# Optimization experiments

Measured on AMD Instinct MI355X. Metric: run time of the kernel, lower is better.

## Reference

```python
import jax, jax.numpy as jnp
import numpy as np

N, E = 3000, 96000
IN_C, HID, OUT_C = 512, 256, 64
K1, K2, K3 = 2000, 1000, 500  # ceil(ratio * n) per depth; ratios = [2000/N, 0.5, 0.5]


def gcn_conv(A, x, W, b):
    # GCNConv(improved=True): A_hat = A + 2I, symmetric norm; A[i, j] = weight of edge j -> i
    n = A.shape[0]
    Ah = A + 2.0 * jnp.eye(n, dtype=A.dtype)
    deg = Ah.sum(axis=1)
    dis = jnp.where(deg > 0, jax.lax.rsqrt(deg), 0.0)
    return (dis[:, None] * Ah * dis[None, :]) @ (x @ W) + b


def augment(A):
    # GraphUNet.augment_adj: add self loops, A @ A (spspmm), remove self loops
    n = A.shape[0]
    eye = jnp.eye(n, dtype=A.dtype)
    Ah = A + eye
    return (Ah @ Ah) * (1.0 - eye)


def topk_pool(A, x, w, k):
    # TopKPooling: score = tanh((x @ w) / ||w||); keep top-k nodes, scale feats, take sub-adjacency
    score = jnp.tanh((x @ w) / jnp.linalg.norm(w))
    sv, perm = jax.lax.top_k(score, k)
    return x[perm] * sv[:, None], A[perm][:, perm], perm


def setup_inputs():
    key = jax.random.key(0)
    ks = jax.random.split(key, 16)

    def glorot(k, shape):
        lim = float(np.sqrt(6.0 / (shape[0] + shape[1])))
        return jax.random.uniform(k, shape, jnp.float32, -lim, lim)

    return {
        "x": jax.random.normal(ks[0], (N, IN_C), jnp.float32),
        "edge_index": jax.random.randint(ks[1], (2, E), 0, N, jnp.int32),
        "W0": glorot(ks[2], (IN_C, HID)), "b0": jnp.zeros((HID,), jnp.float32),
        "W1": glorot(ks[3], (HID, HID)), "b1": jnp.zeros((HID,), jnp.float32),
        "W2": glorot(ks[4], (HID, HID)), "b2": jnp.zeros((HID,), jnp.float32),
        "W3": glorot(ks[5], (HID, HID)), "b3": jnp.zeros((HID,), jnp.float32),
        "p1": jax.random.normal(ks[6], (HID,), jnp.float32),
        "p2": jax.random.normal(ks[7], (HID,), jnp.float32),
        "p3": jax.random.normal(ks[8], (HID,), jnp.float32),
        "U0": glorot(ks[9], (HID, HID)), "c0": jnp.zeros((HID,), jnp.float32),
        "U1": glorot(ks[10], (HID, HID)), "c1": jnp.zeros((HID,), jnp.float32),
        "U2": glorot(ks[11], (HID, OUT_C)), "c2": jnp.zeros((OUT_C,), jnp.float32),
    }


def reference(x, edge_index, W0, b0, W1, b1, W2, b2, W3, b3, p1, p2, p3, U0, c0, U1, c1, U2, c2):
    # eval mode: dropout_edge(p=0.2) and F.dropout(p=0.92) are identity
    relu = jax.nn.relu
    src, dst = edge_index[0], edge_index[1]
    A = jnp.zeros((N, N), x.dtype).at[dst, src].add(1.0)  # dense adjacency, coalesces duplicates

    x0 = relu(gcn_conv(A, x, W0, b0))                     # down conv 0 on original graph
    x1in, A1, perm1 = topk_pool(augment(A), x0, p1, K1)
    x1 = relu(gcn_conv(A1, x1in, W1, b1))
    x2in, A2, perm2 = topk_pool(augment(A1), x1, p2, K2)
    x2 = relu(gcn_conv(A2, x2in, W2, b2))
    x3in, A3, perm3 = topk_pool(augment(A2), x2, p3, K3)
    x3 = relu(gcn_conv(A3, x3in, W3, b3))

    h = x2 + jnp.zeros_like(x2).at[perm3].set(x3)         # unpool + sum residual
    h = relu(gcn_conv(A2, h, U0, c0))
    h = x1 + jnp.zeros_like(x1).at[perm2].set(h)
    h = relu(gcn_conv(A1, h, U1, c1))
    h = x0 + jnp.zeros_like(x0).at[perm1].set(h)
    h = gcn_conv(A, h, U2, c2)                            # final up conv, no activation
    return jax.nn.log_softmax(h, axis=1)
```

## Files before the change

### kernel.cpp

```cpp
#include <hip/hip_runtime.h>
#include <math.h>
#include <stdint.h>

#define N0   3000
#define NE   96000
#define INC  512
#define HIDF 256
#define OUTC 64
#define KP1  2000
#define KP2  1000
#define KP3  500
#define KP1P 2048
#define KP2P 1024
#define KP3P 512

typedef __bf16 bf16x8 __attribute__((ext_vector_type(8)));
typedef float f32x4 __attribute__((ext_vector_type(4)));

#define GLDS16(gp, lp)                                                   \
  __builtin_amdgcn_global_load_lds(                                      \
      (__attribute__((address_space(1))) void*)(gp),                     \
      (__attribute__((address_space(3))) void*)(lp), 16, 0, 0)

static __global__ void count_k(const int* __restrict__ ei, int* __restrict__ cd) {
  int e = blockIdx.x * blockDim.x + threadIdx.x;
  if (e < NE) atomicAdd(&cd[ei[NE + e]], 1);
}

static __global__ __launch_bounds__(1024) void scan_excl_k(const int* __restrict__ cnt,
                                                           int* __restrict__ start, int n,
                                                           float* __restrict__ dis0) {
  __shared__ int s[4096];
  int tid = threadIdx.x;
  for (int i = tid; i < 4096; i += blockDim.x) s[i] = (i < n) ? cnt[i] : 0;
  __syncthreads();
  for (int d = 1; d < 4096; d <<= 1) {
    int v[4]; int r = 0;
    for (int i = tid; i < 4096; i += blockDim.x, ++r) v[r] = (i >= d) ? s[i - d] : 0;
    __syncthreads();
    r = 0;
    for (int i = tid; i < 4096; i += blockDim.x, ++r) s[i] += v[r];
    __syncthreads();
  }
  for (int i = tid; i < n; i += blockDim.x) {
    start[i] = (i == 0) ? 0 : s[i - 1];
    dis0[i] = rsqrtf((float)cnt[i] + 2.0f);
  }
  if (tid == 0) start[n] = s[n - 1];
}

static __global__ void scatter_k(const int* __restrict__ ei, const int* __restrict__ sd,
                                 int* __restrict__ fd, int* __restrict__ bd) {
  int e = blockIdx.x * blockDim.x + threadIdx.x;
  if (e < NE) {
    int d = ei[NE + e];
    bd[sd[d] + atomicAdd(&fd[d], 1)] = ei[e];
  }
}

static __global__ __launch_bounds__(256) void augA_masked_k(
    const int* __restrict__ st, const int* __restrict__ bk,
    const int* __restrict__ perm, const int* __restrict__ pos,
    __bf16* __restrict__ A1bf, float* __restrict__ dis1) {
  __shared__ float row[KP1];
  __shared__ float sh[4];
  int tid = threadIdx.x, lane = tid & 63, wave = tid >> 6;
  int r = blockIdx.x;
  int vi = perm[r];
  for (int c = tid; c < KP1; c += 256) row[c] = 0.f;
  __syncthreads();
  int b = st[vi], e = st[vi + 1];
  for (int t = b + wave; t < e; t += 4) {
    int k = bk[t];
    int jb = st[k], je = st[k + 1];
    for (int u = jb + lane; u < je; u += 64) {
      int p = pos[bk[u]];
      if (p >= 0) atomicAdd(&row[p], 1.0f);
    }
  }
  if (wave == 0)
    for (int t = b + lane; t < e; t += 64) {
      int p = pos[bk[t]];
      if (p >= 0) atomicAdd(&row[p], 2.0f);
    }
  __syncthreads();
  if (tid == 0) row[r] = 0.f;
  __syncthreads();
  float s = 0.f;
  for (int c = tid; c < KP1P; c += 256) {
    float v = (c < KP1) ? row[c] : 0.f;
    A1bf[(size_t)r * KP1P + c] = (__bf16)v;
    s += v;
  }
#pragma unroll
  for (int o = 32; o > 0; o >>= 1) s += __shfl_down(s, o, 64);
  if (lane == 0) sh[wave] = s;
  __syncthreads();
  if (tid == 0) dis1[r] = rsqrtf(sh[0] + sh[1] + sh[2] + sh[3] + 2.0f);
}

static __global__ void spmm_sc_k(const int* __restrict__ start, const int* __restrict__ idx,
                                 const float* __restrict__ xw, const float* __restrict__ dis,
                                 float* __restrict__ out, int F) {
  int row = blockIdx.x;
  int b = start[row], e = start[row + 1];
  int f = threadIdx.x;
  __shared__ int nb[256];
  __shared__ float nd[256];
  float acc = 0.f;
  for (int t0 = b; t0 < e; t0 += blockDim.x) {
    int m = min((int)blockDim.x, e - t0);
    __syncthreads();
    if (f < m) { int s = idx[t0 + f]; nb[f] = s; nd[f] = dis[s]; }
    __syncthreads();
    for (int t = 0; t < m; ++t) acc += xw[(size_t)nb[t] * F + f] * nd[t];
  }
  out[(size_t)row * F + f] = acc;
}

static __global__ void conv_hilo_k(const float* __restrict__ in, int R, int C, int Cp,
                                   __bf16* __restrict__ oh, __bf16* __restrict__ ol) {
  int idx = blockIdx.x * blockDim.x + threadIdx.x;
  if (idx < R * Cp) {
    int r = idx / Cp, c = idx - r * Cp;
    float v = (c < C) ? in[(size_t)r * C + c] : 0.f;
    __bf16 h = (__bf16)v;
    oh[idx] = h;
    if (ol) ol[idx] = (__bf16)(v - (float)h);
  }
}

struct TDesc { const float* in; __bf16* oh; __bf16* ol; int R, C, Rp; };
struct TDescs { TDesc d[7]; };
static __global__ __launch_bounds__(256) void wtconv_k(TDescs ds) {
  TDesc d = ds.d[blockIdx.z];
  int r0 = blockIdx.x * 32, c0 = blockIdx.y * 32;
  if (r0 >= d.Rp || c0 >= d.C) return;
  __shared__ float t[32][33];
  int lr = threadIdx.x >> 5, lc = threadIdx.x & 31;
#pragma unroll
  for (int i = 0; i < 4; ++i) {
    int r = r0 + lr + i * 8, c = c0 + lc;
    t[lr + i * 8][lc] = (r < d.R && c < d.C) ? d.in[(size_t)r * d.C + c] : 0.f;
  }
  __syncthreads();
#pragma unroll
  for (int i = 0; i < 4; ++i) {
    int c = c0 + lr + i * 8, r = r0 + lc;
    if (c < d.C) {
      float v = t[lc][lr + i * 8];
      __bf16 h = (__bf16)v;
      d.oh[(size_t)c * d.Rp + r] = h;
      d.ol[(size_t)c * d.Rp + r] = (__bf16)(v - (float)h);
    }
  }
}

static __global__ __launch_bounds__(256) void btrans_k(const __bf16* __restrict__ ih,
                                                       const __bf16* __restrict__ il,
                                                       __bf16* __restrict__ oh, __bf16* __restrict__ ol,
                                                       int Rin, int Ls, int Cout, int Lo) {
  __shared__ __bf16 th[32][40], tl[32][40];
  int r0 = blockIdx.x * 32, c0 = blockIdx.y * 32;
  int lr = threadIdx.x >> 5, lc = threadIdx.x & 31;
#pragma unroll
  for (int i = 0; i < 4; ++i) {
    int r = r0 + lr + i * 8, c = c0 + lc;
    bool ok = (r < Rin);
    th[lr + i * 8][lc] = ok ? ih[(size_t)r * Ls + c] : (__bf16)0.f;
    if (il) tl[lr + i * 8][lc] = ok ? il[(size_t)r * Ls + c] : (__bf16)0.f;
  }
  __syncthreads();
#pragma unroll
  for (int i = 0; i < 4; ++i) {
    int c = c0 + lr + i * 8, r = r0 + lc;
    if (c < Cout) {
      oh[(size_t)c * Lo + r] = th[lc][lr + i * 8];
      if (ol) ol[(size_t)c * Lo + r] = tl[lc][lr + i * 8];
    }
  }
}

static __global__ __launch_bounds__(256) void redtconv_k(const float* __restrict__ Cp, int ks, int mn,
                                                         int R, int C, int Rp,
                                                         __bf16* __restrict__ oh, __bf16* __restrict__ ol,
                                                         const float* __restrict__ disv,
                                                         float* __restrict__ xw_out) {
  __shared__ float t[32][33];
  int r0 = blockIdx.x * 32, c0 = blockIdx.y * 32;
  int lr = threadIdx.x >> 5, lc = threadIdx.x & 31;
#pragma unroll
  for (int i = 0; i < 4; ++i) {
    int r = r0 + lr + i * 8, c = c0 + lc;
    float v = 0.f;
    if (r < R && c < C) {
      size_t idx = (size_t)r * C + c;
      for (int z = 0; z < ks; ++z) v += Cp[(size_t)z * mn + idx];
      xw_out[idx] = v;
    }
    t[lr + i * 8][lc] = v;
  }
  __syncthreads();
#pragma unroll
  for (int i = 0; i < 4; ++i) {
    int c = c0 + lr + i * 8, r = r0 + lc;
    if (c < C) {
      float v = t[lc][lr + i * 8];
      if (r < R) v *= disv[r];
      __bf16 h = (__bf16)v;
      oh[(size_t)c * Rp + r] = h;
      ol[(size_t)c * Rp + r] = (__bf16)(v - (float)h);
    }
  }
}

static __global__ void ghilo_k(const float* __restrict__ src, const int* __restrict__ perm,
                               const float* __restrict__ sv, __bf16* __restrict__ oh,
                               __bf16* __restrict__ ol, int k) {
  int idx = blockIdx.x * blockDim.x + threadIdx.x;
  if (idx < k * HIDF) {
    int r = idx >> 8;
    float v = src[(size_t)perm[r] * HIDF + (idx & 255)] * sv[r];
    __bf16 h = (__bf16)v;
    oh[idx] = h;
    ol[idx] = (__bf16)(v - (float)h);
  }
}

template <int BM, int BN>
static __global__ __launch_bounds__(256) void mgemm_k(
    const __bf16* __restrict__ A0, const __bf16* __restrict__ A1g, const __bf16* __restrict__ A2g,
    const __bf16* __restrict__ B0, const __bf16* __restrict__ B1g, const __bf16* __restrict__ B2g,
    const int* __restrict__ pA, const int* __restrict__ pB,
    int nseg, float* __restrict__ Cp, int M, int N, int Kp, int kchunk) {
  constexpr int FM = BM / 32, FN = BN / 32;
  __shared__ __bf16 As[2][BM * 64];
  __shared__ __bf16 Bs[2][BN * 64];
  int tid = threadIdx.x;
  int lane = tid & 63, wave = tid >> 6;
  int wx = wave & 1, wy = wave >> 1;
  int l15 = lane & 15, l4 = lane >> 4;
  int brow = blockIdx.y * BM, bcol = blockIdx.x * BN;
  int wrow = wy * (BM / 2), wcol = wx * (BN / 2);
  int srow = lane >> 3, slot = lane & 7;
  int k_beg = blockIdx.z * kchunk;
  int ksteps = kchunk >> 6;
  int nsteps = nseg * ksteps;
  const __bf16* segA[3] = {A0, A1g, A2g};
  const __bf16* segB[3] = {B0, B1g, B2g};

  auto stage = [&](int buf, int t) {
    int seg = t / ksteps;
    int k0 = k_beg + ((t - seg * ksteps) << 6);
    const __bf16* Ag = segA[seg];
    const __bf16* Bg = segB[seg];
#pragma unroll
    for (int i = 0; i < BM / 32; ++i) {
      int rl = (i * 4 + wave) * 8 + srow;
      int gr = brow + rl;
      if (gr >= M) gr = M - 1;
      if (pA) gr = pA[gr];
      int col = k0 + ((slot ^ (rl & 7)) << 3);
      GLDS16(Ag + (size_t)gr * Kp + col, &As[buf][(i * 4 + wave) * 8 * 64]);
    }
#pragma unroll
    for (int i = 0; i < BN / 32; ++i) {
      int rl = (i * 4 + wave) * 8 + srow;
      int gc = bcol + rl;
      if (gc >= N) gc = N - 1;
      if (pB) gc = pB[gc];
      int col = k0 + ((slot ^ (rl & 7)) << 3);
      GLDS16(Bg + (size_t)gc * Kp + col, &Bs[buf][(i * 4 + wave) * 8 * 64]);
    }
  };

  f32x4 acc[FM][FN] = {};
  stage(0, 0);
  __syncthreads();
  int cur = 0;
  for (int t = 0; t < nsteps; ++t) {
    if (t + 1 < nsteps) stage(cur ^ 1, t + 1);
#pragma unroll
    for (int sub = 0; sub < 2; ++sub) {
      bf16x8 af[FM], bfv[FN];
#pragma unroll
      for (int i = 0; i < FM; ++i) {
        int r = wrow + i * 16 + l15;
        af[i] = *(const bf16x8*)(&As[cur][r * 64 + (((sub * 4 + l4) ^ (r & 7)) << 3)]);
      }
#pragma unroll
      for (int j = 0; j < FN; ++j) {
        int r = wcol + j * 16 + l15;
        bfv[j] = *(const bf16x8*)(&Bs[cur][r * 64 + (((sub * 4 + l4) ^ (r & 7)) << 3)]);
      }
#pragma unroll
      for (int i = 0; i < FM; ++i)
#pragma unroll
        for (int j = 0; j < FN; ++j)
          acc[i][j] = __builtin_amdgcn_mfma_f32_16x16x32_bf16(af[i], bfv[j], acc[i][j], 0, 0, 0);
    }
    __syncthreads();
    cur ^= 1;
  }
  size_t zoff = (size_t)blockIdx.z * M * N;
#pragma unroll
  for (int i = 0; i < FM; ++i)
#pragma unroll
    for (int j = 0; j < FN; ++j) {
      int col = bcol + wcol + j * 16 + l15;
      if (col < N) {
#pragma unroll
        for (int q = 0; q < 4; ++q) {
          int row = brow + wrow + i * 16 + l4 * 4 + q;
          if (row < M) Cp[zoff + (size_t)row * N + col] = acc[i][j][q];
        }
      }
    }
}

static __global__ void reduce_k(const float* __restrict__ p, int ks, int mn, float* __restrict__ out) {
  int idx = blockIdx.x * blockDim.x + threadIdx.x;
  if (idx < mn) {
    float s = 0.f;
    for (int z = 0; z < ks; ++z) s += p[(size_t)z * mn + idx];
    out[idx] = s;
  }
}

static __global__ __launch_bounds__(256) void epi_score_k(
    const float* __restrict__ zp, int ks, int mn, const float* __restrict__ xw,
    const float* __restrict__ disv, const float* __restrict__ bias,
    const float* __restrict__ p, float* __restrict__ outx, float* __restrict__ sc) {
  int r = blockIdx.x, tid = threadIdx.x;
  size_t idx = (size_t)r * HIDF + tid;
  float zv = 0.f;
  for (int z = 0; z < ks; ++z) zv += zp[(size_t)z * mn + idx];
  float di = disv[r];
  float v = di * zv + 2.0f * di * di * xw[idx] + bias[tid];
  v = fmaxf(v, 0.0f);
  outx[idx] = v;
  float wv = p[tid];
  float s = v * wv, q = wv * wv;
  __shared__ float sh[4], sh2[4];
  int lane = tid & 63, wid = tid >> 6;
#pragma unroll
  for (int o = 32; o > 0; o >>= 1) { s += __shfl_down(s, o, 64); q += __shfl_down(q, o, 64); }
  if (lane == 0) { sh[wid] = s; sh2[wid] = q; }
  __syncthreads();
  if (tid == 0)
    sc[r] = tanhf((sh[0] + sh[1] + sh[2] + sh[3]) / sqrtf(sh2[0] + sh2[1] + sh2[2] + sh2[3]));
}

static __global__ void unpool_epi_k(const float* __restrict__ base, const float* __restrict__ zp,
                                    int ks, int mn, const float* __restrict__ xwp,
                                    const float* __restrict__ disv, const float* __restrict__ bias,
                                    const int* __restrict__ pos, __bf16* __restrict__ oh,
                                    __bf16* __restrict__ ol, int n) {
  int idx = blockIdx.x * blockDim.x + threadIdx.x;
  if (idx < n * HIDF) {
    int i = idx >> 8, j = idx & 255;
    int p = pos[i];
    float v = base[idx];
    if (p >= 0) {
      size_t pidx = (size_t)p * HIDF + j;
      float zv = 0.f;
      for (int z = 0; z < ks; ++z) zv += zp[(size_t)z * mn + pidx];
      float di = disv[p];
      float u = di * zv + 2.0f * di * di * xwp[pidx] + bias[j];
      v += fmaxf(u, 0.0f);
    }
    __bf16 h = (__bf16)v;
    oh[idx] = h;
    ol[idx] = (__bf16)(v - (float)h);
  }
}

static __global__ __launch_bounds__(256) void aug_epi_k(
    const float* __restrict__ Cp, int ks, int mn, int n, int dstL,
    const __bf16* __restrict__ srcH, const __bf16* __restrict__ srcL, int srcLen,
    const int* __restrict__ permv, __bf16* __restrict__ bh, __bf16* __restrict__ bl,
    float* __restrict__ dis) {
  __shared__ int pm[1000];
  __shared__ float srow[2048];
  __shared__ float sh[4];
  int r = blockIdx.x;
  int tid = threadIdx.x, lane = tid & 63, wave = tid >> 6;
  int vi = permv[r];
  for (int c = tid; c < n; c += 256) pm[c] = permv[c];
  for (int k = tid; k < srcLen; k += 256) {
    float v = (float)srcH[(size_t)vi * srcLen + k];
    if (srcL) v += (float)srcL[(size_t)vi * srcLen + k];
    srow[k] = v;
  }
  __syncthreads();
  float ssum = 0.f;
  for (int c = tid; c < dstL; c += 256) {
    float v = 0.f;
    if (c < n && c != r) {
      for (int z = 0; z < ks; ++z) v += Cp[(size_t)z * mn + (size_t)r * n + c];
      v += 2.0f * srow[pm[c]];
    }
    __bf16 h = (__bf16)v;
    bh[(size_t)r * dstL + c] = h;
    bl[(size_t)r * dstL + c] = (__bf16)(v - (float)h);
    ssum += v;
  }
#pragma unroll
  for (int o = 32; o > 0; o >>= 1) ssum += __shfl_down(ssum, o, 64);
  if (lane == 0) sh[wave] = ssum;
  __syncthreads();
  if (tid == 0) dis[r] = rsqrtf(sh[0] + sh[1] + sh[2] + sh[3] + 2.0f);
}

static __global__ __launch_bounds__(256) void topk_rank_k(const float* __restrict__ sc, int n, int k,
                                                          int* __restrict__ perm, float* __restrict__ sv,
                                                          int* __restrict__ pos) {
  __shared__ float s[N0 + 8];
  int tid = threadIdx.x, lane = tid & 63, wave = tid >> 6;
  for (int i = tid; i < n; i += 256) s[i] = sc[i];
  __syncthreads();
  int i = blockIdx.x * 4 + wave;
  if (i < n) {
    float si = s[i];
    int rank = 0;
    for (int j = lane; j < n; j += 64) {
      float sj = s[j];
      rank += (sj > si) || (sj == si && j < i);
    }
#pragma unroll
    for (int o = 32; o > 0; o >>= 1) rank += __shfl_down(rank, o, 64);
    if (lane == 0) {
      pos[i] = (rank < k) ? rank : -1;
      if (rank < k) { perm[rank] = i; sv[rank] = si; }
    }
  }
}

static __global__ void epilsm_k(const float* __restrict__ zb, const float* __restrict__ xw,
                                const float* __restrict__ dis, const float* __restrict__ b,
                                float* __restrict__ out) {
  int r = blockIdx.x, j = threadIdx.x;
  float di = dis[r];
  float v = di * zb[r * OUTC + j] + 2.0f * di * di * xw[r * OUTC + j] + b[j];
  float m = v;
#pragma unroll
  for (int o = 32; o > 0; o >>= 1) m = fmaxf(m, __shfl_xor(m, o, 64));
  float e = expf(v - m), s = e;
#pragma unroll
  for (int o = 32; o > 0; o >>= 1) s += __shfl_xor(s, o, 64);
  out[r * OUTC + j] = v - m - logf(s);
}

extern "C" void kernel_launch(void* const* d_in, const int* in_sizes, int n_in,
                              void* d_out, int out_size, void* d_ws, size_t ws_size,
                              hipStream_t stream) {
  const float* x  = (const float*)d_in[0];
  const int* ei   = (const int*)d_in[1];
  const float* W0 = (const float*)d_in[2];
  const float* b0 = (const float*)d_in[3];
  const float* W1 = (const float*)d_in[4];
  const float* b1 = (const float*)d_in[5];
  const float* W2 = (const float*)d_in[6];
  const float* b2 = (const float*)d_in[7];
  const float* W3 = (const float*)d_in[8];
  const float* b3 = (const float*)d_in[9];
  const float* p1 = (const float*)d_in[10];
  const float* p2 = (const float*)d_in[11];
  const float* p3 = (const float*)d_in[12];
  const float* U0 = (const float*)d_in[13];
  const float* c0 = (const float*)d_in[14];
  const float* U1 = (const float*)d_in[15];
  const float* c1 = (const float*)d_in[16];
  const float* U2 = (const float*)d_in[17];
  const float* c2 = (const float*)d_in[18];
  (void)in_sizes; (void)n_in; (void)out_size; (void)ws_size;

  char* basep = (char*)d_ws;
  size_t off = 0;
  auto alloc = [&](size_t bytes) {
    void* p = basep + off;
    off += (bytes + 255) & ~(size_t)255;
    return p;
  };

  float* xw  = (float*)alloc((size_t)N0 * HIDF * 4);
  float* zb  = (float*)alloc((size_t)N0 * HIDF * 4);
  float* x0  = (float*)alloc((size_t)N0 * HIDF * 4);
  float* x1  = (float*)alloc((size_t)KP1 * HIDF * 4);
  float* x2  = (float*)alloc((size_t)KP2 * HIDF * 4);
  float* Cpart = (float*)alloc((size_t)20 * 1024 * 1024);
  __bf16* bfAh = (__bf16*)alloc((size_t)N0 * INC * 2);
  __bf16* bfAl = (__bf16*)alloc((size_t)N0 * INC * 2);
  __bf16* bfBh = (__bf16*)alloc((size_t)HIDF * KP1P * 2);
  __bf16* bfBl = (__bf16*)alloc((size_t)HIDF * KP1P * 2);
  __bf16* A1bf  = (__bf16*)alloc((size_t)KP1 * KP1P * 2);
  __bf16* A1tbf = (__bf16*)alloc((size_t)KP1 * KP1P * 2);
  __bf16* A2bh  = (__bf16*)alloc((size_t)KP2 * KP2P * 2);
  __bf16* A2bl  = (__bf16*)alloc((size_t)KP2 * KP2P * 2);
  __bf16* A2tbh = (__bf16*)alloc((size_t)KP2 * KP2P * 2);
  __bf16* A2tbl = (__bf16*)alloc((size_t)KP2 * KP2P * 2);
  __bf16* A3bh  = (__bf16*)alloc((size_t)KP3 * KP3P * 2);
  __bf16* A3bl  = (__bf16*)alloc((size_t)KP3 * KP3P * 2);
  __bf16* w0h = (__bf16*)alloc((size_t)HIDF * 512 * 2);
  __bf16* w0l = (__bf16*)alloc((size_t)HIDF * 512 * 2);
  __bf16* w1h = (__bf16*)alloc((size_t)HIDF * 256 * 2);
  __bf16* w1l = (__bf16*)alloc((size_t)HIDF * 256 * 2);
  __bf16* w2h = (__bf16*)alloc((size_t)HIDF * 256 * 2);
  __bf16* w2l = (__bf16*)alloc((size_t)HIDF * 256 * 2);
  __bf16* w3h = (__bf16*)alloc((size_t)HIDF * 256 * 2);
  __bf16* w3l = (__bf16*)alloc((size_t)HIDF * 256 * 2);
  __bf16* u0h = (__bf16*)alloc((size_t)HIDF * 256 * 2);
  __bf16* u0l = (__bf16*)alloc((size_t)HIDF * 256 * 2);
  __bf16* u1h = (__bf16*)alloc((size_t)HIDF * 256 * 2);
  __bf16* u1l = (__bf16*)alloc((size_t)HIDF * 256 * 2);
  __bf16* u2h = (__bf16*)alloc((size_t)OUTC * 256 * 2);
  __bf16* u2l = (__bf16*)alloc((size_t)OUTC * 256 * 2);
  float* sc   = (float*)alloc(N0 * 4);
  float* sv   = (float*)alloc(KP1 * 4);
  int* perm1  = (int*)alloc(KP1 * 4);
  int* perm2  = (int*)alloc(KP2 * 4);
  int* perm3  = (int*)alloc(KP3 * 4);
  int* pos1   = (int*)alloc(N0 * 4);
  int* pos2   = (int*)alloc(KP1 * 4);
  int* pos3   = (int*)alloc(KP2 * 4);
  float* dis0 = (float*)alloc(N0 * 4);
  float* dis1 = (float*)alloc(KP1 * 4);
  float* dis2 = (float*)alloc(KP2 * 4);
  float* dis3 = (float*)alloc(KP3 * 4);
  int* cf     = (int*)alloc((size_t)2 * 3072 * 4);
  int* cnt_d  = cf;
  int* fl_d   = cf + 3072;
  int* st_d   = (int*)alloc((N0 + 4) * 4);
  int* bk_d   = (int*)alloc(NE * 4);

  auto mg = [&](int bm, int bn, const __bf16* a0, const __bf16* a1, const __bf16* a2,
                const __bf16* bb0, const __bf16* bb1, const __bf16* bb2,
                const int* pA, const int* pB,
                int nseg, int M, int N, int Kp, int ks, int kchunk) {
    dim3 g((N + bn - 1) / bn, (M + bm - 1) / bm, ks);
    if (bm == 128 && bn == 128)
      mgemm_k<128, 128><<<g, 256, 0, stream>>>(a0, a1, a2, bb0, bb1, bb2, pA, pB, nseg, Cpart, M, N, Kp, kchunk);
    else if (bm == 128)
      mgemm_k<128, 64><<<g, 256, 0, stream>>>(a0, a1, a2, bb0, bb1, bb2, pA, pB, nseg, Cpart, M, N, Kp, kchunk);
    else
      mgemm_k<64, 64><<<g, 256, 0, stream>>>(a0, a1, a2, bb0, bb1, bb2, pA, pB, nseg, Cpart, M, N, Kp, kchunk);
  };

  auto wgemm = [&](const __bf16* wh, const __bf16* wl, int fin, int fout, int n, int bm,
                   int ks, int kchunk) {
    int Kp = (fin + 63) & ~63;
    mg(bm, 64, bfAh, bfAh, bfAl, wh, wl, wh, nullptr, nullptr, 3, n, fout, Kp, ks, kchunk);
  };

  auto propg = [&](int ksw, const __bf16* Abh, const __bf16* Abl, int asegs, int n, int Kp, int bm,
                   int ks, int kchunk, const float* disv) {
    dim3 tg(Kp / 32, HIDF / 32);
    redtconv_k<<<tg, 256, 0, stream>>>(Cpart, ksw, n * HIDF, n, HIDF, Kp, bfBh, bfBl, disv, xw);
    if (asegs == 1) mg(bm, 64, Abh, Abh, nullptr, bfBh, bfBl, nullptr, nullptr, nullptr, 2, n, HIDF, Kp, ks, kchunk);
    else            mg(bm, 64, Abh, Abh, Abl, bfBh, bfBl, bfBh, nullptr, nullptr, 3, n, HIDF, Kp, ks, kchunk);
  };

  hipMemsetAsync(cf, 0, (size_t)2 * 3072 * 4, stream);
  count_k<<<(NE + 255) / 256, 256, 0, stream>>>(ei, cnt_d);
  {
    TDescs ds;
    ds.d[0] = {W0, w0h, w0l, INC, HIDF, 512};
    ds.d[1] = {W1, w1h, w1l, HIDF, HIDF, 256};
    ds.d[2] = {W2, w2h, w2l, HIDF, HIDF, 256};
    ds.d[3] = {W3, w3h, w3l, HIDF, HIDF, 256};
    ds.d[4] = {U0, u0h, u0l, HIDF, HIDF, 256};
    ds.d[5] = {U1, u1h, u1l, HIDF, HIDF, 256};
    ds.d[6] = {U2, u2h, u2l, HIDF, OUTC, 256};
    wtconv_k<<<dim3(16, 8, 7), 256, 0, stream>>>(ds);
  }
  scan_excl_k<<<1, 1024, 0, stream>>>(cnt_d, st_d, N0, dis0);
  scatter_k<<<(NE + 255) / 256, 256, 0, stream>>>(ei, st_d, fl_d, bk_d);

  conv_hilo_k<<<((size_t)N0 * INC + 255) / 256, 256, 0, stream>>>(x, N0, INC, INC, bfAh, bfAl);
  wgemm(w0h, w0l, INC, HIDF, N0, 128, 4, 128);
  reduce_k<<<(N0 * HIDF + 255) / 256, 256, 0, stream>>>(Cpart, 4, N0 * HIDF, xw);
  spmm_sc_k<<<N0, HIDF, 0, stream>>>(st_d, bk_d, xw, dis0, zb, HIDF);
  epi_score_k<<<N0, 256, 0, stream>>>(zb, 1, 0, xw, dis0, b0, p1, x0, sc);
  topk_rank_k<<<(N0 + 3) / 4, 256, 0, stream>>>(sc, N0, KP1, perm1, sv, pos1);

  augA_masked_k<<<KP1, 256, 0, stream>>>(st_d, bk_d, perm1, pos1, A1bf, dis1);

  ghilo_k<<<((size_t)KP1 * HIDF + 255) / 256, 256, 0, stream>>>(x0, perm1, sv, bfAh, bfAl, KP1);
  wgemm(w1h, w1l, HIDF, HIDF, KP1, 128, 4, 64);
  propg(4, A1bf, nullptr, 1, KP1, KP1P, 128, 4, 512, dis1);
  epi_score_k<<<KP1, 256, 0, stream>>>(Cpart, 4, KP1 * HIDF, xw, dis1, b1, p2, x1, sc);
  topk_rank_k<<<(KP1 + 3) / 4, 256, 0, stream>>>(sc, KP1, KP2, perm2, sv, pos2);

  btrans_k<<<dim3(KP1P / 32, (KP1 + 31) / 32), 256, 0, stream>>>(A1bf, nullptr, A1tbf, nullptr,
                                                                 KP1, KP1P, KP1, KP1P);
  mg(128, 128, A1bf, nullptr, nullptr, A1tbf, nullptr, nullptr, perm2, perm2,
     1, KP2, KP2, KP1P, 4, 512);
  aug_epi_k<<<KP2, 256, 0, stream>>>(Cpart, 4, KP2 * KP2, KP2, KP2P, A1bf, nullptr, KP1P, perm2,
                                     A2bh, A2bl, dis2);

  ghilo_k<<<((size_t)KP2 * HIDF + 255) / 256, 256, 0, stream>>>(x1, perm2, sv, bfAh, bfAl, KP2);
  wgemm(w2h, w2l, HIDF, HIDF, KP2, 64, 4, 64);
  propg(4, A2bh, A2bl, 2, KP2, KP2P, 128, 8, 128, dis2);
  epi_score_k<<<KP2, 256, 0, stream>>>(Cpart, 8, KP2 * HIDF, xw, dis2, b2, p3, x2, sc);
  topk_rank_k<<<(KP2 + 3) / 4, 256, 0, stream>>>(sc, KP2, KP3, perm3, sv, pos3);

  btrans_k<<<dim3(KP2P / 32, (KP2 + 31) / 32), 256, 0, stream>>>(A2bh, A2bl, A2tbh, A2tbl,
                                                                 KP2, KP2P, KP2, KP2P);
  mg(64, 64, A2bh, A2bh, A2bl, A2tbh, A2tbl, A2tbh, perm3, perm3, 3, KP3, KP3, KP2P, 4, 256);
  aug_epi_k<<<KP3, 256, 0, stream>>>(Cpart, 4, KP3 * KP3, KP3, KP3P, A2bh, A2bl, KP2P, perm3,
                                     A3bh, A3bl, dis3);

  ghilo_k<<<((size_t)KP3 * HIDF + 255) / 256, 256, 0, stream>>>(x2, perm3, sv, bfAh, bfAl, KP3);
  wgemm(w3h, w3l, HIDF, HIDF, KP3, 64, 4, 64);
  propg(4, A3bh, A3bl, 2, KP3, KP3P, 64, 8, 64, dis3);
  unpool_epi_k<<<(KP2 * HIDF + 255) / 256, 256, 0, stream>>>(x2, Cpart, 8, KP3 * HIDF, xw, dis3, b3,
                                                             pos3, bfAh, bfAl, KP2);

  wgemm(u0h, u0l, HIDF, HIDF, KP2, 64, 4, 64);
  propg(4, A2bh, A2bl, 2, KP2, KP2P, 128, 8, 128, dis2);
  unpool_epi_k<<<(KP1 * HIDF + 255) / 256, 256, 0, stream>>>(x1, Cpart, 8, KP2 * HIDF, xw, dis2, c0,
                                                             pos2, bfAh, bfAl, KP1);

  wgemm(u1h, u1l, HIDF, HIDF, KP1, 128, 4, 64);
  propg(4, A1bf, nullptr, 1, KP1, KP1P, 128, 4, 512, dis1);
  unpool_epi_k<<<(N0 * HIDF + 255) / 256, 256, 0, stream>>>(x0, Cpart, 4, KP1 * HIDF, xw, dis1, c1,
                                                            pos1, bfAh, bfAl, N0);

  wgemm(u2h, u2l, HIDF, OUTC, N0, 64, 4, 64);
  reduce_k<<<(N0 * OUTC + 255) / 256, 256, 0, stream>>>(Cpart, 4, N0 * OUTC, xw);
  spmm_sc_k<<<N0, OUTC, 0, stream>>>(st_d, bk_d, xw, dis0, zb, OUTC);
  epilsm_k<<<N0, OUTC, 0, stream>>>(zb, xw, dis0, c2, (float*)d_out);
}
```

Baseline: 450.5 us.

## Drop split-K for weight GEMMs, hoist gathered row indices, reduce split factors

Weight GEMMs now run without split-K (64x64 tiles, full K) and write straight into xw, which removes the separate reduce_k kernels and the partial-sum traffic. The redtconv kernel then reads xw directly. Permuted row and column indices in the GEMM are computed once per block rather than at every stage. Split-K factors for the propagation and augmentation GEMMs are cut from 8 or 4 down to 4 or 2, with larger k-chunks. The trade-off is fewer blocks, so less parallelism, on small problems in exchange for less reduction work and fewer launches.

Result: no change. 459.1 us (+1.9%).

```diff
diff --git a/kernel.cpp b/kernel.cpp
--- a/kernel.cpp
+++ b/kernel.cpp
@@ -196,7 +196,7 @@
     if (r < R && c < C) {
       size_t idx = (size_t)r * C + c;
       for (int z = 0; z < ks; ++z) v += Cp[(size_t)z * mn + idx];
-      xw_out[idx] = v;
+      if (xw_out) xw_out[idx] = v;
     }
     t[lr + i * 8][lc] = v;
   }
@@ -249,6 +249,22 @@
   const __bf16* segA[3] = {A0, A1g, A2g};
   const __bf16* segB[3] = {B0, B1g, B2g};
 
+  int rowA[BM / 32], rowB[BN / 32];
+#pragma unroll
+  for (int i = 0; i < BM / 32; ++i) {
+    int rl = (i * 4 + wave) * 8 + srow;
+    int gr = brow + rl;
+    if (gr >= M) gr = M - 1;
+    rowA[i] = pA ? pA[gr] : gr;
+  }
+#pragma unroll
+  for (int i = 0; i < BN / 32; ++i) {
+    int rl = (i * 4 + wave) * 8 + srow;
+    int gc = bcol + rl;
+    if (gc >= N) gc = N - 1;
+    rowB[i] = pB ? pB[gc] : gc;
+  }
+
   auto stage = [&](int buf, int t) {
     int seg = t / ksteps;
     int k0 = k_beg + ((t - seg * ksteps) << 6);
@@ -257,20 +273,14 @@
 #pragma unroll
     for (int i = 0; i < BM / 32; ++i) {
       int rl = (i * 4 + wave) * 8 + srow;
-      int gr = brow + rl;
-      if (gr >= M) gr = M - 1;
-      if (pA) gr = pA[gr];
       int col = k0 + ((slot ^ (rl & 7)) << 3);
-      GLDS16(Ag + (size_t)gr * Kp + col, &As[buf][(i * 4 + wave) * 8 * 64]);
+      GLDS16(Ag + (size_t)rowA[i] * Kp + col, &As[buf][(i * 4 + wave) * 8 * 64]);
     }
 #pragma unroll
     for (int i = 0; i < BN / 32; ++i) {
       int rl = (i * 4 + wave) * 8 + srow;
-      int gc = bcol + rl;
-      if (gc >= N) gc = N - 1;
-      if (pB) gc = pB[gc];
       int col = k0 + ((slot ^ (rl & 7)) << 3);
-      GLDS16(Bg + (size_t)gc * Kp + col, &Bs[buf][(i * 4 + wave) * 8 * 64]);
+      GLDS16(Bg + (size_t)rowB[i] * Kp + col, &Bs[buf][(i * 4 + wave) * 8 * 64]);
     }
   };
 
@@ -316,15 +326,6 @@
         }
       }
     }
-}
-
-static __global__ void reduce_k(const float* __restrict__ p, int ks, int mn, float* __restrict__ out) {
-  int idx = blockIdx.x * blockDim.x + threadIdx.x;
-  if (idx < mn) {
-    float s = 0.f;
-    for (int z = 0; z < ks; ++z) s += p[(size_t)z * mn + idx];
-    out[idx] = s;
-  }
 }
 
 static __global__ __launch_bounds__(256) void epi_score_k(
@@ -535,29 +536,28 @@
 
   auto mg = [&](int bm, int bn, const __bf16* a0, const __bf16* a1, const __bf16* a2,
                 const __bf16* bb0, const __bf16* bb1, const __bf16* bb2,
-                const int* pA, const int* pB,
-                int nseg, int M, int N, int Kp, int ks, int kchunk) {
+                const int* pA, const int* pB, int nseg, float* Cdst,
+                int M, int N, int Kp, int ks, int kchunk) {
     dim3 g((N + bn - 1) / bn, (M + bm - 1) / bm, ks);
     if (bm == 128 && bn == 128)
-      mgemm_k<128, 128><<<g, 256, 0, stream>>>(a0, a1, a2, bb0, bb1, bb2, pA, pB, nseg, Cpart, M, N, Kp, kchunk);
+      mgemm_k<128, 128><<<g, 256, 0, stream>>>(a0, a1, a2, bb0, bb1, bb2, pA, pB, nseg, Cdst, M, N, Kp, kchunk);
     else if (bm == 128)
-      mgemm_k<128, 64><<<g, 256, 0, stream>>>(a0, a1, a2, bb0, bb1, bb2, pA, pB, nseg, Cpart, M, N, Kp, kchunk);
+      mgemm_k<128, 64><<<g, 256, 0, stream>>>(a0, a1, a2, bb0, bb1, bb2, pA, pB, nseg, Cdst, M, N, Kp, kchunk);
     else
-      mgemm_k<64, 64><<<g, 256, 0, stream>>>(a0, a1, a2, bb0, bb1, bb2, pA, pB, nseg, Cpart, M, N, Kp, kchunk);
+      mgemm_k<64, 64><<<g, 256, 0, stream>>>(a0, a1, a2, bb0, bb1, bb2, pA, pB, nseg, Cdst, M, N, Kp, kchunk);
   };
 
-  auto wgemm = [&](const __bf16* wh, const __bf16* wl, int fin, int fout, int n, int bm,
-                   int ks, int kchunk) {
+  auto wgemm = [&](const __bf16* wh, const __bf16* wl, int fin, int fout, int n) {
     int Kp = (fin + 63) & ~63;
-    mg(bm, 64, bfAh, bfAh, bfAl, wh, wl, wh, nullptr, nullptr, 3, n, fout, Kp, ks, kchunk);
+    mg(64, 64, bfAh, bfAh, bfAl, wh, wl, wh, nullptr, nullptr, 3, xw, n, fout, Kp, 1, Kp);
   };
 
-  auto propg = [&](int ksw, const __bf16* Abh, const __bf16* Abl, int asegs, int n, int Kp, int bm,
+  auto propg = [&](const __bf16* Abh, const __bf16* Abl, int asegs, int n, int Kp, int bm,
                    int ks, int kchunk, const float* disv) {
     dim3 tg(Kp / 32, HIDF / 32);
-    redtconv_k<<<tg, 256, 0, stream>>>(Cpart, ksw, n * HIDF, n, HIDF, Kp, bfBh, bfBl, disv, xw);
-    if (asegs == 1) mg(bm, 64, Abh, Abh, nullptr, bfBh, bfBl, nullptr, nullptr, nullptr, 2, n, HIDF, Kp, ks, kchunk);
-    else            mg(bm, 64, Abh, Abh, Abl, bfBh, bfBl, bfBh, nullptr, nullptr, 3, n, HIDF, Kp, ks, kchunk);
+    redtconv_k<<<tg, 256, 0, stream>>>(xw, 1, 0, n, HIDF, Kp, bfBh, bfBl, disv, nullptr);
+    if (asegs == 1) mg(bm, 64, Abh, Abh, nullptr, bfBh, bfBl, nullptr, nullptr, nullptr, 2, Cpart, n, HIDF, Kp, ks, kchunk);
+    else            mg(bm, 64, Abh, Abh, Abl, bfBh, bfBl, bfBh, nullptr, nullptr, 3, Cpart, n, HIDF, Kp, ks, kchunk);
   };
 
   hipMemsetAsync(cf, 0, (size_t)2 * 3072 * 4, stream);
@@ -577,8 +577,7 @@
   scatter_k<<<(NE + 255) / 256, 256, 0, stream>>>(ei, st_d, fl_d, bk_d);
 
   conv_hilo_k<<<((size_t)N0 * INC + 255) / 256, 256, 0, stream>>>(x, N0, INC, INC, bfAh, bfAl);
-  wgemm(w0h, w0l, INC, HIDF, N0, 128, 4, 128);
-  reduce_k<<<(N0 * HIDF + 255) / 256, 256, 0, stream>>>(Cpart, 4, N0 * HIDF, xw);
+  wgemm(w0h, w0l, INC, HIDF, N0);
   spmm_sc_k<<<N0, HIDF, 0, stream>>>(st_d, bk_d, xw, dis0, zb, HIDF);
   epi_score_k<<<N0, 256, 0, stream>>>(zb, 1, 0, xw, dis0, b0, p1, x0, sc);
   topk_rank_k<<<(N0 + 3) / 4, 256, 0, stream>>>(sc, N0, KP1, perm1, sv, pos1);
@@ -586,48 +585,47 @@
   augA_masked_k<<<KP1, 256, 0, stream>>>(st_d, bk_d, perm1, pos1, A1bf, dis1);
 
   ghilo_k<<<((size_t)KP1 * HIDF + 255) / 256, 256, 0, stream>>>(x0, perm1, sv, bfAh, bfAl, KP1);
-  wgemm(w1h, w1l, HIDF, HIDF, KP1, 128, 4, 64);
-  propg(4, A1bf, nullptr, 1, KP1, KP1P, 128, 4, 512, dis1);
+  wgemm(w1h, w1l, HIDF, HIDF, KP1);
+  propg(A1bf, nullptr, 1, KP1, KP1P, 128, 4, 512, dis1);
   epi_score_k<<<KP1, 256, 0, stream>>>(Cpart, 4, KP1 * HIDF, xw, dis1, b1, p2, x1, sc);
   topk_rank_k<<<(KP1 + 3) / 4, 256, 0, stream>>>(sc, KP1, KP2, perm2, sv, pos2);
 
   btrans_k<<<dim3(KP1P / 32, (KP1 + 31) / 32), 256, 0, stream>>>(A1bf, nullptr, A1tbf, nullptr,
                                                                  KP1, KP1P, KP1, KP1P);
   mg(128, 128, A1bf, nullptr, nullptr, A1tbf, nullptr, nullptr, perm2, perm2,
-     1, KP2, KP2, KP1P, 4, 512);
-  aug_epi_k<<<KP2, 256, 0, stream>>>(Cpart, 4, KP2 * KP2, KP2, KP2P, A1bf, nullptr, KP1P, perm2,
+     1, Cpart, KP2, KP2, KP1P, 2, 1024);
+  aug_epi_k<<<KP2, 256, 0, stream>>>(Cpart, 2, KP2 * KP2, KP2, KP2P, A1bf, nullptr, KP1P, perm2,
                                      A2bh, A2bl, dis2);
 
   ghilo_k<<<((size_t)KP2 * HIDF + 255) / 256, 256, 0, stream>>>(x1, perm2, sv, bfAh, bfAl, KP2);
-  wgemm(w2h, w2l, HIDF, HIDF, KP2, 64, 4, 64);
-  propg(4, A2bh, A2bl, 2, KP2, KP2P, 128, 8, 128, dis2);
-  epi_score_k<<<KP2, 256, 0, stream>>>(Cpart, 8, KP2 * HIDF, xw, dis2, b2, p3, x2, sc);
+  wgemm(w2h, w2l, HIDF, HIDF, KP2);
+  propg(A2bh, A2bl, 2, KP2, KP2P, 128, 4, 256, dis2);
+  epi_score_k<<<KP2, 256, 0, stream>>>(Cpart, 4, KP2 * HIDF, xw, dis2, b2, p3, x2, sc);
   topk_rank_k<<<(KP2 + 3) / 4, 256, 0, stream>>>(sc, KP2, KP3, perm3, sv, pos3);
 
   btrans_k<<<dim3(KP2P / 32, (KP2 + 31) / 32), 256, 0, stream>>>(A2bh, A2bl, A2tbh, A2tbl,
                                                                  KP2, KP2P, KP2, KP2P);
-  mg(64, 64, A2bh, A2bh, A2bl, A2tbh, A2tbl, A2tbh, perm3, perm3, 3, KP3, KP3, KP2P, 4, 256);
-  aug_epi_k<<<KP3, 256, 0, stream>>>(Cpart, 4, KP3 * KP3, KP3, KP3P, A2bh, A2bl, KP2P, perm3,
+  mg(64, 64, A2bh, A2bh, A2bl, A2tbh, A2tbl, A2tbh, perm3, perm3, 3, Cpart, KP3, KP3, KP2P, 2, 512);
+  aug_epi_k<<<KP3, 256, 0, stream>>>(Cpart, 2, KP3 * KP3, KP3, KP3P, A2bh, A2bl, KP2P, perm3,
                                      A3bh, A3bl, dis3);
 
   ghilo_k<<<((size_t)KP3 * HIDF + 255) / 256, 256, 0, stream>>>(x2, perm3, sv, bfAh, bfAl, KP3);
-  wgemm(w3h, w3l, HIDF, HIDF, KP3, 64, 4, 64);
-  propg(4, A3bh, A3bl, 2, KP3, KP3P, 64, 8, 64, dis3);
-  unpool_epi_k<<<(KP2 * HIDF + 255) / 256, 256, 0, stream>>>(x2, Cpart, 8, KP3 * HIDF, xw, dis3, b3,
+  wgemm(w3h, w3l, HIDF, HIDF, KP3);
+  propg(A3bh, A3bl, 2, KP3, KP3P, 64, 4, 128, dis3);
+  unpool_epi_k<<<(KP2 * HIDF + 255) / 256, 256, 0, stream>>>(x2, Cpart, 4, KP3 * HIDF, xw, dis3, b3,
                                                              pos3, bfAh, bfAl, KP2);
 
-  wgemm(u0h, u0l, HIDF, HIDF, KP2, 64, 4, 64);
-  propg(4, A2bh, A2bl, 2, KP2, KP2P, 128, 8, 128, dis2);
-  unpool_epi_k<<<(KP1 * HIDF + 255) / 256, 256, 0, stream>>>(x1, Cpart, 8, KP2 * HIDF, xw, dis2, c0,
+  wgemm(u0h, u0l, HIDF, HIDF, KP2);
+  propg(A2bh, A2bl, 2, KP2, KP2P, 128, 4, 256, dis2);
+  unpool_epi_k<<<(KP1 * HIDF + 255) / 256, 256, 0, stream>>>(x1, Cpart, 4, KP2 * HIDF, xw, dis2, c0,
                                                              pos2, bfAh, bfAl, KP1);
 
-  wgemm(u1h, u1l, HIDF, HIDF, KP1, 128, 4, 64);
-  propg(4, A1bf, nullptr, 1, KP1, KP1P, 128, 4, 512, dis1);
+  wgemm(u1h, u1l, HIDF, HIDF, KP1);
+  propg(A1bf, nullptr, 1, KP1, KP1P, 128, 4, 512, dis1);
   unpool_epi_k<<<(N0 * HIDF + 255) / 256, 256, 0, stream>>>(x0, Cpart, 4, KP1 * HIDF, xw, dis1, c1,
                                                             pos1, bfAh, bfAl, N0);
 
-  wgemm(u2h, u2l, HIDF, OUTC, N0, 64, 4, 64);
-  reduce_k<<<(N0 * OUTC + 255) / 256, 256, 0, stream>>>(Cpart, 4, N0 * OUTC, xw);
+  wgemm(u2h, u2l, HIDF, OUTC, N0);
   spmm_sc_k<<<N0, OUTC, 0, stream>>>(st_d, bk_d, xw, dis0, zb, OUTC);
   epilsm_k<<<N0, OUTC, 0, stream>>>(zb, xw, dis0, c2, (float*)d_out);
 }
```
